# Kernel optimization log

Measured on AMD Instinct MI355X. Metric: run time of the kernel, lower is better.

## Reference

```python
import jax, jax.numpy as jnp
import numpy as np

K_ORDER = 3
GRID_N = 10
GRID_LO, GRID_HI = -2.0, 2.0
LAYERS = [(49, 256), (256, 256), (256, 10)]
NCOEF = GRID_N + K_ORDER  # 13


def mish(x):
    return x * jnp.tanh(jax.nn.softplus(x))


def bspline_basis(x):
    # x: (B, in) -> basis (B, in, GRID_N + K_ORDER)
    h = (GRID_HI - GRID_LO) / GRID_N
    knots = GRID_LO + h * jnp.arange(-K_ORDER, GRID_N + K_ORDER + 1, dtype=x.dtype)  # (G+2k+1,)
    xx = x[..., None]
    B = ((xx >= knots[:-1]) & (xx < knots[1:])).astype(x.dtype)  # degree-0, (B,in,G+2k)
    for d in range(1, K_ORDER + 1):
        left = (xx - knots[: -(d + 1)]) / (knots[d:-1] - knots[: -(d + 1)]) * B[..., :-1]
        right = (knots[d + 1:] - xx) / (knots[d + 1:] - knots[1:-d]) * B[..., 1:]
        B = left + right
    return B  # (B, in, G+k)


def kan_layer(x, coef, scale_base, scale_sp, bias):
    # x: (B,in); coef: (in,out,G+k); scales: (in,out); bias: (out,)
    basis = bspline_basis(x)                                   # (B,in,G+k)
    spline = jnp.einsum('big,iog->bo', basis, coef * scale_sp[..., None])
    base = jnp.einsum('bi,io->bo', mish(x), scale_base)
    return base + spline + bias


def setup_inputs() -> dict:
    key = jax.random.key(0)
    ks = jax.random.split(key, 1 + 4 * len(LAYERS))
    inp = {'x': jax.random.normal(ks[0], (8192, 1, 28, 28), dtype=jnp.float32)}
    i = 1
    for li, (fin, fout) in enumerate(LAYERS, start=1):
        inp[f'coef{li}'] = 0.1 * jax.random.normal(ks[i], (fin, fout, NCOEF), dtype=jnp.float32); i += 1
        inp[f'sb{li}'] = 1.0 + 0.1 * jax.random.normal(ks[i], (fin, fout), dtype=jnp.float32); i += 1
        inp[f'sp{li}'] = 1.0 + 0.1 * jax.random.normal(ks[i], (fin, fout), dtype=jnp.float32); i += 1
        inp[f'b{li}'] = jnp.zeros((fout,), dtype=jnp.float32); i += 1
    return inp


def reference(x, coef1, sb1, sp1, b1, coef2, sb2, sp2, b2, coef3, sb3, sp3, b3):
    B = x.shape[0]
    # avg_pool2d(x, 4): 28x28 -> 7x7
    h = x.reshape(B, 1, 7, 4, 7, 4).mean(axis=(3, 5))
    h = h.reshape(B, 49)
    h = kan_layer(h, coef1, sb1, sp1, b1)
    h = kan_layer(h, coef2, sb2, sp2, b2)
    h = kan_layer(h, coef3, sb3, sp3, b3)
    return jax.nn.log_softmax(h, axis=1)
```

## Files before the change

### kernel.cpp

```cpp
#include <hip/hip_runtime.h>
#include <hip/hip_bf16.h>

typedef __bf16 bf16x8_t __attribute__((ext_vector_type(8)));
typedef float f32x4_t __attribute__((ext_vector_type(4)));
using bf16 = __hip_bfloat16;

__device__ __forceinline__ unsigned short f2bf_bits(float v) {
  __hip_bfloat16 h = __float2bfloat16(v);
  return *reinterpret_cast<unsigned short*>(&h);
}

__device__ __forceinline__ float mish_f(float x) {
  float z = __expf(x);
  float n = z * (z + 2.0f);
  float m = x * n / (n + 2.0f);
  return (x > 10.0f) ? x : m;
}

__device__ __forceinline__ void kan_feats28(bf16* dst, float x) {
  unsigned int* d32 = (unsigned int*)dst;
#pragma unroll
  for (int d = 0; d < 7; ++d) d32[d] = 0u;
  float t = (x + 3.2f) * 2.5f;
  if (t >= 0.0f && t < 16.0f) {
    float tf = floorf(t);
    int c = (int)tf;
    float u = t - tf;
    float um = 1.0f - u;
    float u2 = u * u, u3 = u2 * u;
    const float s6 = 1.0f / 6.0f;
    float w0 = um * um * um * s6;
    float w1 = (3.0f * u3 - 6.0f * u2 + 4.0f) * s6;
    float w2 = (-3.0f * u3 + 3.0f * u2 + 3.0f * u + 1.0f) * s6;
    float w3 = u3 * s6;
    int j0 = c - 3;
    if (j0 >= 0)               dst[j0]     = __float2bfloat16(w0);
    if (j0 >= -1 && j0 <= 11)  dst[j0 + 1] = __float2bfloat16(w1);
    if (j0 >= -2 && j0 <= 10)  dst[j0 + 2] = __float2bfloat16(w2);
    if (j0 <= 9)               dst[j0 + 3] = __float2bfloat16(w3);
  }
  dst[13] = __float2bfloat16(mish_f(x));
}

__global__ __launch_bounds__(256) void prep_all(
    const float* __restrict__ c1, const float* __restrict__ sb1, const float* __restrict__ sp1,
    const float* __restrict__ c2, const float* __restrict__ sb2, const float* __restrict__ sp2,
    const float* __restrict__ c3, const float* __restrict__ sb3, const float* __restrict__ sp3,
    bf16* __restrict__ W1f, bf16* __restrict__ W2f, bf16* __restrict__ W3f) {
  const int b = blockIdx.x, o = threadIdx.x;
  float vals[14];
  const int ntg = o >> 4, lrr = o & 15;
  if (b < 49) {
    const int i = b;
    const size_t io = (size_t)i * 256 + o;
    const float spv = sp1[io];
#pragma unroll
    for (int r = 0; r < 13; ++r) vals[r] = c1[io * 13 + r] * spv;
    vals[13] = sb1[io];
#pragma unroll
    for (int d = 0; d < 7; ++d) {
      const int k2 = i * 14 + 2 * d;
      const int s = k2 >> 5, r2 = k2 & 31;
      const size_t off = ((size_t)(s * 16 + ntg)) * 512 + lrr * 32 + (r2 >> 3) * 8 + (r2 & 7);
      *(unsigned int*)(W1f + off) = (unsigned int)f2bf_bits(vals[2 * d]) |
                                    ((unsigned int)f2bf_bits(vals[2 * d + 1]) << 16);
    }
  } else if (b == 49) {
#pragma unroll
    for (int d = 0; d < 9; ++d) {
      const int k2 = 686 + 2 * d;
      const int r2 = k2 & 31;
      *(unsigned int*)(W1f + ((size_t)(21 * 16 + ntg)) * 512 + lrr * 32 + (r2 >> 3) * 8 + (r2 & 7)) = 0u;
    }
  } else if (b < 306) {
    const int i = b - 50;
    const size_t io = (size_t)i * 256 + o;
    const float spv = sp2[io];
#pragma unroll
    for (int r = 0; r < 13; ++r) vals[r] = c2[io * 13 + r] * spv;
    vals[13] = sb2[io];
#pragma unroll
    for (int d = 0; d < 7; ++d) {
      const int k2 = i * 14 + 2 * d;
      const int s = k2 >> 5, r2 = k2 & 31;
      const size_t off = ((size_t)(s * 16 + ntg)) * 512 + lrr * 32 + (r2 >> 3) * 8 + (r2 & 7);
      *(unsigned int*)(W2f + off) = (unsigned int)f2bf_bits(vals[2 * d]) |
                                    ((unsigned int)f2bf_bits(vals[2 * d + 1]) << 16);
    }
  } else {
    const int i = b - 306;
    if (o < 10) {
      const size_t io = (size_t)i * 10 + o;
      const float spv = sp3[io];
#pragma unroll
      for (int r = 0; r < 13; ++r) vals[r] = c3[io * 13 + r] * spv;
      vals[13] = sb3[io];
#pragma unroll
      for (int d = 0; d < 7; ++d) {
        const int k2 = i * 14 + 2 * d;
        const int s = k2 >> 5, r2 = k2 & 31;
        const size_t off = (size_t)s * 512 + o * 32 + (r2 >> 3) * 8 + (r2 & 7);
        *(unsigned int*)(W3f + off) = (unsigned int)f2bf_bits(vals[2 * d]) |
                                      ((unsigned int)f2bf_bits(vals[2 * d + 1]) << 16);
      }
    } else if (o < 16) {
#pragma unroll
      for (int d = 0; d < 7; ++d) {
        const int k2 = i * 14 + 2 * d;
        const int s = k2 >> 5, r2 = k2 & 31;
        *(unsigned int*)(W3f + (size_t)s * 512 + o * 32 + (r2 >> 3) * 8 + (r2 & 7)) = 0u;
      }
    }
  }
}

__global__ __launch_bounds__(512, 2) void meganet(
    const float* __restrict__ x, const bf16* __restrict__ W1f,
    const bf16* __restrict__ W2f, const bf16* __restrict__ W3f,
    const float* __restrict__ b1, const float* __restrict__ b2,
    const float* __restrict__ b3, float* __restrict__ out) {
  __shared__ __align__(16) char lds[120320];
  float* const xs = (float*)lds;
  float* const P = (float*)(lds + 50176);
  float* const Hs1 = (float*)lds;
  bf16* const Ach0 = (bf16*)(lds + 57344);
  bf16* const Ach1 = (bf16*)(lds + 72192);
  float* const Hs2 = (float*)(lds + 87040);
  float* const Red = (float*)lds;
  float* const V = (float*)(lds + 14336);

  const int t = threadIdx.x;
  const int w = t >> 6, lane = t & 63, quad = lane >> 4, lr = lane & 15;
  const int tr = t >> 4, ej = t & 15;
  const int r0 = blockIdx.x * 32;
  const int ntg0 = w * 2;
  const int foff = lr * 32 + quad * 8;

  for (int h = 0; h < 2; ++h) {
    const float4* src = (const float4*)x + (size_t)(r0 + h * 16) * 196;
    float4* xd = (float4*)xs;
#pragma unroll
    for (int l = 0; l < 7; ++l) {
      const int idx = t + l * 512;
      if (idx < 3136) xd[idx] = src[idx];
    }
    __syncthreads();
    for (int task = t; task < 784; task += 512) {
      const int img = task / 49, p = task - img * 49;
      const int oh = p / 7, ow = p - oh * 7;
      const float* xi = xs + img * 784 + oh * 112 + ow * 4;
      float s = 0.f;
#pragma unroll
      for (int rr = 0; rr < 4; ++rr)
#pragma unroll
        for (int cc = 0; cc < 4; ++cc) s += xi[rr * 28 + cc];
      P[(h * 16 + img) * 56 + p] = s * (1.0f / 16.0f);
    }
    __syncthreads();
  }

  f32x4_t acc1[2][2];
#pragma unroll
  for (int m = 0; m < 2; ++m)
#pragma unroll
    for (int n = 0; n < 2; ++n) acc1[m][n] = (f32x4_t){0.f, 0.f, 0.f, 0.f};
  bf16x8_t qa[4], qb[4];
#pragma unroll
  for (int s = 0; s < 4; ++s) {
    qa[s] = *(const bf16x8_t*)(W1f + (size_t)(s * 16 + ntg0) * 512 + foff);
    qb[s] = *(const bf16x8_t*)(W1f + (size_t)(s * 16 + ntg0 + 1) * 512 + foff);
  }
  kan_feats28(Ach0 + tr * 232 + ej * 14, P[tr * 56 + ej]);
  __syncthreads();
#pragma unroll
  for (int c = 0; c < 4; ++c) {
    const bf16* const Ac = (c & 1) ? Ach1 : Ach0;
    bf16* const An = (c & 1) ? Ach0 : Ach1;
    const int nks = (c < 3) ? 7 : 1;
#pragma unroll
    for (int ks = 0; ks < 7; ++ks) {
      if (ks >= nks) continue;
      const int kk = c * 7 + ks;
      const int sl = kk & 3;
      bf16x8_t bb0 = qa[sl], bb1 = qb[sl];
      if (kk + 4 < 22) {
        qa[sl] = *(const bf16x8_t*)(W1f + (size_t)((kk + 4) * 16 + ntg0) * 512 + foff);
        qb[sl] = *(const bf16x8_t*)(W1f + (size_t)((kk + 4) * 16 + ntg0 + 1) * 512 + foff);
      }
#pragma unroll
      for (int m = 0; m < 2; ++m) {
        bf16x8_t a = *(const bf16x8_t*)(Ac + (m * 16 + lr) * 232 + ks * 32 + quad * 8);
        acc1[m][0] = __builtin_amdgcn_mfma_f32_16x16x32_bf16(a, bb0, acc1[m][0], 0, 0, 0);
        acc1[m][1] = __builtin_amdgcn_mfma_f32_16x16x32_bf16(a, bb1, acc1[m][1], 0, 0, 0);
      }
    }
    if (c < 2) {
      kan_feats28(An + tr * 232 + ej * 14, P[tr * 56 + (c + 1) * 16 + ej]);
    } else if (c == 2) {
      if (ej == 0) kan_feats28(An + tr * 232, P[tr * 56 + 48]);
      else if (ej == 1) {
        unsigned int* z = (unsigned int*)(An + tr * 232 + 14);
#pragma unroll
        for (int d = 0; d < 9; ++d) z[d] = 0u;
      }
    }
    __syncthreads();
  }
#pragma unroll
  for (int m = 0; m < 2; ++m)
#pragma unroll
    for (int n = 0; n < 2; ++n) {
      const int col = w * 32 + n * 16 + lr;
      const float bn = b1[col];
#pragma unroll
      for (int r = 0; r < 4; ++r)
        Hs1[(m * 16 + quad * 4 + r) * 260 + col] = acc1[m][n][r] + bn;
    }
  __syncthreads();

  f32x4_t acc2[2][2];
#pragma unroll
  for (int m = 0; m < 2; ++m)
#pragma unroll
    for (int n = 0; n < 2; ++n) acc2[m][n] = (f32x4_t){0.f, 0.f, 0.f, 0.f};
#pragma unroll
  for (int s = 0; s < 4; ++s) {
    qa[s] = *(const bf16x8_t*)(W2f + (size_t)(s * 16 + ntg0) * 512 + foff);
    qb[s] = *(const bf16x8_t*)(W2f + (size_t)(s * 16 + ntg0 + 1) * 512 + foff);
  }
  kan_feats28(Ach0 + tr * 232 + ej * 14, Hs1[tr * 260 + ej]);
  __syncthreads();
#pragma unroll
  for (int c = 0; c < 16; ++c) {
    const bf16* const Ac = (c & 1) ? Ach1 : Ach0;
    bf16* const An = (c & 1) ? Ach0 : Ach1;
#pragma unroll
    for (int ks = 0; ks < 7; ++ks) {
      const int kk = c * 7 + ks;
      const int sl = kk & 3;
      bf16x8_t bb0 = qa[sl], bb1 = qb[sl];
      if (kk + 4 < 112) {
        qa[sl] = *(const bf16x8_t*)(W2f + (size_t)((kk + 4) * 16 + ntg0) * 512 + foff);
        qb[sl] = *(const bf16x8_t*)(W2f + (size_t)((kk + 4) * 16 + ntg0 + 1) * 512 + foff);
      }
#pragma unroll
      for (int m = 0; m < 2; ++m) {
        bf16x8_t a = *(const bf16x8_t*)(Ac + (m * 16 + lr) * 232 + ks * 32 + quad * 8);
        acc2[m][0] = __builtin_amdgcn_mfma_f32_16x16x32_bf16(a, bb0, acc2[m][0], 0, 0, 0);
        acc2[m][1] = __builtin_amdgcn_mfma_f32_16x16x32_bf16(a, bb1, acc2[m][1], 0, 0, 0);
      }
    }
    if (c < 15)
      kan_feats28(An + tr * 232 + ej * 14, Hs1[tr * 260 + (c + 1) * 16 + ej]);
    __syncthreads();
  }
#pragma unroll
  for (int m = 0; m < 2; ++m)
#pragma unroll
    for (int n = 0; n < 2; ++n) {
      const int col = w * 32 + n * 16 + lr;
      const float bn = b2[col];
#pragma unroll
      for (int r = 0; r < 4; ++r)
        Hs2[(m * 16 + quad * 4 + r) * 260 + col] = acc2[m][n][r] + bn;
    }
  __syncthreads();

  f32x4_t acc3[2];
  acc3[0] = (f32x4_t){0.f, 0.f, 0.f, 0.f};
  acc3[1] = acc3[0];
  bf16x8_t w3q[2];
  if (w < 7) {
    w3q[0] = *(const bf16x8_t*)(W3f + (size_t)(0 * 7 + w) * 512 + foff);
    w3q[1] = *(const bf16x8_t*)(W3f + (size_t)(1 * 7 + w) * 512 + foff);
  }
  kan_feats28(Ach0 + tr * 232 + ej * 14, Hs2[tr * 260 + ej]);
  __syncthreads();
#pragma unroll
  for (int c = 0; c < 16; ++c) {
    const bf16* const Ac = (c & 1) ? Ach1 : Ach0;
    bf16* const An = (c & 1) ? Ach0 : Ach1;
    if (w < 7) {
      bf16x8_t bb = w3q[c & 1];
      if (c + 2 < 16)
        w3q[c & 1] = *(const bf16x8_t*)(W3f + (size_t)((c + 2) * 7 + w) * 512 + foff);
#pragma unroll
      for (int m = 0; m < 2; ++m) {
        bf16x8_t a = *(const bf16x8_t*)(Ac + (m * 16 + lr) * 232 + w * 32 + quad * 8);
        acc3[m] = __builtin_amdgcn_mfma_f32_16x16x32_bf16(a, bb, acc3[m], 0, 0, 0);
      }
    }
    if (c < 15)
      kan_feats28(An + tr * 232 + ej * 14, Hs2[tr * 260 + (c + 1) * 16 + ej]);
    __syncthreads();
  }
  if (w < 7) {
#pragma unroll
    for (int m = 0; m < 2; ++m)
#pragma unroll
      for (int r = 0; r < 4; ++r)
        Red[w * 512 + (m * 16 + quad * 4 + r) * 16 + lr] = acc3[m][r];
  }
  __syncthreads();
  {
    float s = (ej < 10) ? b3[ej] : 0.f;
#pragma unroll
    for (int wv = 0; wv < 7; ++wv) s += Red[wv * 512 + tr * 16 + ej];
    V[tr * 16 + ej] = s;
  }
  __syncthreads();
  if (t < 32) {
    float vv[10];
#pragma unroll
    for (int o = 0; o < 10; ++o) vv[o] = V[t * 16 + o];
    float mx = vv[0];
#pragma unroll
    for (int o = 1; o < 10; ++o) mx = fmaxf(mx, vv[o]);
    float se = 0.f;
#pragma unroll
    for (int o = 0; o < 10; ++o) se += expf(vv[o] - mx);
    const float l = mx + logf(se);
#pragma unroll
    for (int o = 0; o < 10; ++o) out[(size_t)(r0 + t) * 10 + o] = vv[o] - l;
  }
}

extern "C" void kernel_launch(void* const* d_in, const int* in_sizes, int n_in,
                              void* d_out, int out_size, void* d_ws, size_t ws_size,
                              hipStream_t stream) {
  const float* x = (const float*)d_in[0];
  const float* coef1 = (const float*)d_in[1];
  const float* sb1 = (const float*)d_in[2];
  const float* sp1 = (const float*)d_in[3];
  const float* b1 = (const float*)d_in[4];
  const float* coef2 = (const float*)d_in[5];
  const float* sb2 = (const float*)d_in[6];
  const float* sp2 = (const float*)d_in[7];
  const float* b2 = (const float*)d_in[8];
  const float* coef3 = (const float*)d_in[9];
  const float* sb3 = (const float*)d_in[10];
  const float* sp3 = (const float*)d_in[11];
  const float* b3 = (const float*)d_in[12];
  float* out = (float*)d_out;

  char* ws = (char*)d_ws;
  bf16* W1f = (bf16*)ws;
  bf16* W2f = (bf16*)(ws + 360448);
  bf16* W3f = (bf16*)(ws + 2195456);

  prep_all<<<562, 256, 0, stream>>>(coef1, sb1, sp1, coef2, sb2, sp2,
                                    coef3, sb3, sp3, W1f, W2f, W3f);
  meganet<<<256, 512, 0, stream>>>(x, W1f, W2f, W3f, b1, b2, b3, out);
}
```

Measured before the change: 141.1 us.

## Double block to 1024 threads, one N-tile per wave, shrink LDS

Each block now runs 16 waves instead of 8, so each wave owns a single 16-column output tile instead of two. Layer 3 splits its M halves across 14 waves. The hidden activations are stored transposed in one shared buffer, cutting LDS from about 120KB to 72KB. The goal is more waves to hide MFMA and load latency, and lower LDS use per block. In exchange, feature generation still uses only half the threads, and the larger block adds barrier cost with the same 256-block grid.

Result: no change. 139.7 us (-1.0%).

```diff
diff --git a/kernel.cpp b/kernel.cpp
--- a/kernel.cpp
+++ b/kernel.cpp
@@ -114,39 +114,37 @@
   }
 }
 
-__global__ __launch_bounds__(512, 2) void meganet(
+__global__ __launch_bounds__(1024, 4) void meganet(
     const float* __restrict__ x, const bf16* __restrict__ W1f,
     const bf16* __restrict__ W2f, const bf16* __restrict__ W3f,
     const float* __restrict__ b1, const float* __restrict__ b2,
     const float* __restrict__ b3, float* __restrict__ out) {
-  __shared__ __align__(16) char lds[120320];
+  __shared__ __align__(16) char lds[73728];
+  float* const Hs = (float*)lds;
+  bf16* const Ach0 = (bf16*)(lds + 36864);
+  bf16* const Ach1 = (bf16*)(lds + 51712);
+  float* const P = (float*)(lds + 66560);
   float* const xs = (float*)lds;
-  float* const P = (float*)(lds + 50176);
-  float* const Hs1 = (float*)lds;
-  bf16* const Ach0 = (bf16*)(lds + 57344);
-  bf16* const Ach1 = (bf16*)(lds + 72192);
-  float* const Hs2 = (float*)(lds + 87040);
-  float* const Red = (float*)lds;
-  float* const V = (float*)(lds + 14336);
+  float* const Red = (float*)(lds + 36864);
+  float* const V = (float*)(lds + 51712);
 
   const int t = threadIdx.x;
   const int w = t >> 6, lane = t & 63, quad = lane >> 4, lr = lane & 15;
   const int tr = t >> 4, ej = t & 15;
   const int r0 = blockIdx.x * 32;
-  const int ntg0 = w * 2;
   const int foff = lr * 32 + quad * 8;
 
   for (int h = 0; h < 2; ++h) {
     const float4* src = (const float4*)x + (size_t)(r0 + h * 16) * 196;
     float4* xd = (float4*)xs;
 #pragma unroll
-    for (int l = 0; l < 7; ++l) {
-      const int idx = t + l * 512;
+    for (int l = 0; l < 4; ++l) {
+      const int idx = t + l * 1024;
       if (idx < 3136) xd[idx] = src[idx];
     }
     __syncthreads();
-    for (int task = t; task < 784; task += 512) {
-      const int img = task / 49, p = task - img * 49;
+    if (t < 784) {
+      const int img = t / 49, p = t - img * 49;
       const int oh = p / 7, ow = p - oh * 7;
       const float* xi = xs + img * 784 + oh * 112 + ow * 4;
       float s = 0.f;
@@ -159,18 +157,14 @@
     __syncthreads();
   }
 
-  f32x4_t acc1[2][2];
-#pragma unroll
-  for (int m = 0; m < 2; ++m)
-#pragma unroll
-    for (int n = 0; n < 2; ++n) acc1[m][n] = (f32x4_t){0.f, 0.f, 0.f, 0.f};
-  bf16x8_t qa[4], qb[4];
-#pragma unroll
-  for (int s = 0; s < 4; ++s) {
-    qa[s] = *(const bf16x8_t*)(W1f + (size_t)(s * 16 + ntg0) * 512 + foff);
-    qb[s] = *(const bf16x8_t*)(W1f + (size_t)(s * 16 + ntg0 + 1) * 512 + foff);
-  }
-  kan_feats28(Ach0 + tr * 232 + ej * 14, P[tr * 56 + ej]);
+  f32x4_t acc1[2];
+  acc1[0] = (f32x4_t){0.f, 0.f, 0.f, 0.f};
+  acc1[1] = acc1[0];
+  bf16x8_t q[4];
+#pragma unroll
+  for (int s = 0; s < 4; ++s)
+    q[s] = *(const bf16x8_t*)(W1f + (size_t)(s * 16 + w) * 512 + foff);
+  if (t < 512) kan_feats28(Ach0 + tr * 232 + ej * 14, P[tr * 56 + ej]);
   __syncthreads();
 #pragma unroll
   for (int c = 0; c < 4; ++c) {
@@ -182,53 +176,49 @@
       if (ks >= nks) continue;
       const int kk = c * 7 + ks;
       const int sl = kk & 3;
-      bf16x8_t bb0 = qa[sl], bb1 = qb[sl];
-      if (kk + 4 < 22) {
-        qa[sl] = *(const bf16x8_t*)(W1f + (size_t)((kk + 4) * 16 + ntg0) * 512 + foff);
-        qb[sl] = *(const bf16x8_t*)(W1f + (size_t)((kk + 4) * 16 + ntg0 + 1) * 512 + foff);
-      }
+      bf16x8_t bb = q[sl];
+      if (kk + 4 < 22)
+        q[sl] = *(const bf16x8_t*)(W1f + (size_t)((kk + 4) * 16 + w) * 512 + foff);
 #pragma unroll
       for (int m = 0; m < 2; ++m) {
         bf16x8_t a = *(const bf16x8_t*)(Ac + (m * 16 + lr) * 232 + ks * 32 + quad * 8);
-        acc1[m][0] = __builtin_amdgcn_mfma_f32_16x16x32_bf16(a, bb0, acc1[m][0], 0, 0, 0);
-        acc1[m][1] = __builtin_amdgcn_mfma_f32_16x16x32_bf16(a, bb1, acc1[m][1], 0, 0, 0);
-      }
-    }
-    if (c < 2) {
-      kan_feats28(An + tr * 232 + ej * 14, P[tr * 56 + (c + 1) * 16 + ej]);
-    } else if (c == 2) {
-      if (ej == 0) kan_feats28(An + tr * 232, P[tr * 56 + 48]);
-      else if (ej == 1) {
-        unsigned int* z = (unsigned int*)(An + tr * 232 + 14);
-#pragma unroll
-        for (int d = 0; d < 9; ++d) z[d] = 0u;
-      }
-    }
-    __syncthreads();
-  }
-#pragma unroll
-  for (int m = 0; m < 2; ++m)
-#pragma unroll
-    for (int n = 0; n < 2; ++n) {
-      const int col = w * 32 + n * 16 + lr;
-      const float bn = b1[col];
-#pragma unroll
-      for (int r = 0; r < 4; ++r)
-        Hs1[(m * 16 + quad * 4 + r) * 260 + col] = acc1[m][n][r] + bn;
-    }
-  __syncthreads();
-
-  f32x4_t acc2[2][2];
-#pragma unroll
-  for (int m = 0; m < 2; ++m)
-#pragma unroll
-    for (int n = 0; n < 2; ++n) acc2[m][n] = (f32x4_t){0.f, 0.f, 0.f, 0.f};
-#pragma unroll
-  for (int s = 0; s < 4; ++s) {
-    qa[s] = *(const bf16x8_t*)(W2f + (size_t)(s * 16 + ntg0) * 512 + foff);
-    qb[s] = *(const bf16x8_t*)(W2f + (size_t)(s * 16 + ntg0 + 1) * 512 + foff);
-  }
-  kan_feats28(Ach0 + tr * 232 + ej * 14, Hs1[tr * 260 + ej]);
+        acc1[m] = __builtin_amdgcn_mfma_f32_16x16x32_bf16(a, bb, acc1[m], 0, 0, 0);
+      }
+    }
+    if (t < 512) {
+      if (c < 2) {
+        kan_feats28(An + tr * 232 + ej * 14, P[tr * 56 + (c + 1) * 16 + ej]);
+      } else if (c == 2) {
+        if (ej == 0) kan_feats28(An + tr * 232, P[tr * 56 + 48]);
+        else if (ej == 1) {
+          unsigned int* z = (unsigned int*)(An + tr * 232 + 14);
+#pragma unroll
+          for (int d = 0; d < 9; ++d) z[d] = 0u;
+        }
+      }
+    }
+    __syncthreads();
+  }
+  {
+    const int col = w * 16 + lr;
+    const float bn = b1[col];
+#pragma unroll
+    for (int m = 0; m < 2; ++m) {
+      f32x4_t v;
+#pragma unroll
+      for (int r = 0; r < 4; ++r) v[r] = acc1[m][r] + bn;
+      *(f32x4_t*)(Hs + col * 36 + m * 16 + quad * 4) = v;
+    }
+  }
+  __syncthreads();
+
+  f32x4_t acc2[2];
+  acc2[0] = (f32x4_t){0.f, 0.f, 0.f, 0.f};
+  acc2[1] = acc2[0];
+#pragma unroll
+  for (int s = 0; s < 4; ++s)
+    q[s] = *(const bf16x8_t*)(W2f + (size_t)(s * 16 + w) * 512 + foff);
+  if (t < 512) kan_feats28(Ach0 + tr * 232 + ej * 14, Hs[ej * 36 + tr]);
   __syncthreads();
 #pragma unroll
   for (int c = 0; c < 16; ++c) {
@@ -238,74 +228,67 @@
     for (int ks = 0; ks < 7; ++ks) {
       const int kk = c * 7 + ks;
       const int sl = kk & 3;
-      bf16x8_t bb0 = qa[sl], bb1 = qb[sl];
-      if (kk + 4 < 112) {
-        qa[sl] = *(const bf16x8_t*)(W2f + (size_t)((kk + 4) * 16 + ntg0) * 512 + foff);
-        qb[sl] = *(const bf16x8_t*)(W2f + (size_t)((kk + 4) * 16 + ntg0 + 1) * 512 + foff);
-      }
+      bf16x8_t bb = q[sl];
+      if (kk + 4 < 112)
+        q[sl] = *(const bf16x8_t*)(W2f + (size_t)((kk + 4) * 16 + w) * 512 + foff);
 #pragma unroll
       for (int m = 0; m < 2; ++m) {
         bf16x8_t a = *(const bf16x8_t*)(Ac + (m * 16 + lr) * 232 + ks * 32 + quad * 8);
-        acc2[m][0] = __builtin_amdgcn_mfma_f32_16x16x32_bf16(a, bb0, acc2[m][0], 0, 0, 0);
-        acc2[m][1] = __builtin_amdgcn_mfma_f32_16x16x32_bf16(a, bb1, acc2[m][1], 0, 0, 0);
-      }
-    }
-    if (c < 15)
-      kan_feats28(An + tr * 232 + ej * 14, Hs1[tr * 260 + (c + 1) * 16 + ej]);
-    __syncthreads();
-  }
-#pragma unroll
-  for (int m = 0; m < 2; ++m)
-#pragma unroll
-    for (int n = 0; n < 2; ++n) {
-      const int col = w * 32 + n * 16 + lr;
-      const float bn = b2[col];
-#pragma unroll
-      for (int r = 0; r < 4; ++r)
-        Hs2[(m * 16 + quad * 4 + r) * 260 + col] = acc2[m][n][r] + bn;
-    }
-  __syncthreads();
-
-  f32x4_t acc3[2];
-  acc3[0] = (f32x4_t){0.f, 0.f, 0.f, 0.f};
-  acc3[1] = acc3[0];
-  bf16x8_t w3q[2];
-  if (w < 7) {
-    w3q[0] = *(const bf16x8_t*)(W3f + (size_t)(0 * 7 + w) * 512 + foff);
-    w3q[1] = *(const bf16x8_t*)(W3f + (size_t)(1 * 7 + w) * 512 + foff);
-  }
-  kan_feats28(Ach0 + tr * 232 + ej * 14, Hs2[tr * 260 + ej]);
+        acc2[m] = __builtin_amdgcn_mfma_f32_16x16x32_bf16(a, bb, acc2[m], 0, 0, 0);
+      }
+    }
+    if (t < 512 && c < 15)
+      kan_feats28(An + tr * 232 + ej * 14, Hs[((c + 1) * 16 + ej) * 36 + tr]);
+    __syncthreads();
+  }
+  {
+    const int col = w * 16 + lr;
+    const float bn = b2[col];
+#pragma unroll
+    for (int m = 0; m < 2; ++m) {
+      f32x4_t v;
+#pragma unroll
+      for (int r = 0; r < 4; ++r) v[r] = acc2[m][r] + bn;
+      *(f32x4_t*)(Hs + col * 36 + m * 16 + quad * 4) = v;
+    }
+  }
+  __syncthreads();
+
+  f32x4_t acc3 = {0.f, 0.f, 0.f, 0.f};
+  const int mh = w / 7, ks3 = w % 7;
+  bf16x8_t q3[2];
+  if (w < 14) {
+    q3[0] = *(const bf16x8_t*)(W3f + (size_t)ks3 * 512 + foff);
+    q3[1] = *(const bf16x8_t*)(W3f + (size_t)(7 + ks3) * 512 + foff);
+  }
+  if (t < 512) kan_feats28(Ach0 + tr * 232 + ej * 14, Hs[ej * 36 + tr]);
   __syncthreads();
 #pragma unroll
   for (int c = 0; c < 16; ++c) {
     const bf16* const Ac = (c & 1) ? Ach1 : Ach0;
     bf16* const An = (c & 1) ? Ach0 : Ach1;
-    if (w < 7) {
-      bf16x8_t bb = w3q[c & 1];
+    if (w < 14) {
+      bf16x8_t bb = q3[c & 1];
       if (c + 2 < 16)
-        w3q[c & 1] = *(const bf16x8_t*)(W3f + (size_t)((c + 2) * 7 + w) * 512 + foff);
-#pragma unroll
-      for (int m = 0; m < 2; ++m) {
-        bf16x8_t a = *(const bf16x8_t*)(Ac + (m * 16 + lr) * 232 + w * 32 + quad * 8);
-        acc3[m] = __builtin_amdgcn_mfma_f32_16x16x32_bf16(a, bb, acc3[m], 0, 0, 0);
-      }
-    }
-    if (c < 15)
-      kan_feats28(An + tr * 232 + ej * 14, Hs2[tr * 260 + (c + 1) * 16 + ej]);
-    __syncthreads();
-  }
-  if (w < 7) {
-#pragma unroll
-    for (int m = 0; m < 2; ++m)
-#pragma unroll
-      for (int r = 0; r < 4; ++r)
-        Red[w * 512 + (m * 16 + quad * 4 + r) * 16 + lr] = acc3[m][r];
-  }
-  __syncthreads();
-  {
+        q3[c & 1] = *(const bf16x8_t*)(W3f + (size_t)((c + 2) * 7 + ks3) * 512 + foff);
+      bf16x8_t a = *(const bf16x8_t*)(Ac + (mh * 16 + lr) * 232 + ks3 * 32 + quad * 8);
+      acc3 = __builtin_amdgcn_mfma_f32_16x16x32_bf16(a, bb, acc3, 0, 0, 0);
+    }
+    if (t < 512 && c < 15)
+      kan_feats28(An + tr * 232 + ej * 14, Hs[((c + 1) * 16 + ej) * 36 + tr]);
+    __syncthreads();
+  }
+  if (w < 14) {
+#pragma unroll
+    for (int r = 0; r < 4; ++r)
+      Red[w * 256 + (quad * 4 + r) * 16 + lr] = acc3[r];
+  }
+  __syncthreads();
+  if (t < 512 && tr < 32) {
     float s = (ej < 10) ? b3[ej] : 0.f;
-#pragma unroll
-    for (int wv = 0; wv < 7; ++wv) s += Red[wv * 512 + tr * 16 + ej];
+    const int mh2 = tr >> 4, lrow = tr & 15;
+#pragma unroll
+    for (int ks = 0; ks < 7; ++ks) s += Red[(mh2 * 7 + ks) * 256 + lrow * 16 + ej];
     V[tr * 16 + ej] = s;
   }
   __syncthreads();
@@ -350,5 +333,5 @@
 
   prep_all<<<562, 256, 0, stream>>>(coef1, sb1, sp1, coef2, sb2, sp2,
                                     coef3, sb3, sp3, W1f, W2f, W3f);
-  meganet<<<256, 512, 0, stream>>>(x, W1f, W2f, W3f, b1, b2, b3, out);
-}
+  meganet<<<256, 1024, 0, stream>>>(x, W1f, W2f, W3f, b1, b2, b3, out);
+}
```
